# Optimization experiments

Hardware: AMD Instinct MI355X
Metric: run time of the kernel (lower is better)

## Reference

```python
import jax, jax.numpy as jnp
import numpy as np

N = 300000   # active voxels
K = 27       # 3^3 kernel offsets (kernel_size=3, D=3)
CIN = 64
COUT = 96
EPS = 1e-5   # MinkowskiBatchNorm default eps


def setup_inputs() -> dict:
    key = jax.random.key(0)
    ks = jax.random.split(key, 4)
    x = jax.random.normal(ks[0], (N, CIN), jnp.float32)
    nbrs = jax.random.randint(ks[1], (N, K), 0, N, jnp.int32)
    W1 = jax.random.normal(ks[2], (K, CIN, COUT), jnp.float32) * (1.0 / np.sqrt(K * CIN))
    W2 = jax.random.normal(ks[3], (K, COUT, COUT), jnp.float32) * (1.0 / np.sqrt(K * COUT))
    g1 = jnp.ones((COUT,), jnp.float32)
    b1 = jnp.zeros((COUT,), jnp.float32)
    g2 = jnp.ones((COUT,), jnp.float32)
    b2 = jnp.zeros((COUT,), jnp.float32)
    return {"x": x, "nbrs": nbrs, "W1": W1, "g1": g1, "b1": b1,
            "W2": W2, "g2": g2, "b2": b2}


def _sparse_conv(x, nbrs, W):
    # x: [N, Cin], nbrs: [N, K], W: [K, Cin, Cout]
    # Gather-GEMM-scatter with identical in/out coords (stride-1 3^D conv):
    # out[i] = sum_k x[nbrs[i,k]] @ W[k]. Scan over K to avoid the [N,K,Cin] blowup.
    acc0 = jnp.zeros((x.shape[0], W.shape[-1]), x.dtype)
    def step(acc, kw):
        nbr_k, W_k = kw
        return acc + x[nbr_k] @ W_k, None
    acc, _ = jax.lax.scan(step, acc0, (nbrs.T, W))
    return acc


def _bn_relu(h, gamma, beta):
    # training-mode batch norm over the point axis, then ReLU
    mu = jnp.mean(h, axis=0)
    var = jnp.var(h, axis=0)
    return jax.nn.relu((h - mu) * jax.lax.rsqrt(var + EPS) * gamma + beta)


def reference(x, nbrs, W1, g1, b1, W2, g2, b2):
    h = _bn_relu(_sparse_conv(x, nbrs, W1), g1, b1)
    return _bn_relu(_sparse_conv(h, nbrs, W2), g2, b2)
```

## Files before the change

### kernel.cpp

```cpp
#include <hip/hip_runtime.h>
#include <hip/hip_bf16.h>
#include <stdint.h>

#define N_VOX 300000
#define KNB   27
#define COUT  96
#define EPS   1e-5f
#define BM    256
#define NBLK  ((N_VOX + BM - 1) / BM)
#define QS_H  (255.0f / 6.0f)
#define XCLAMP 4.2f
#define QS_X  (127.0f / XCLAMP)

typedef __attribute__((ext_vector_type(8))) short  short8;
typedef __attribute__((ext_vector_type(4))) float  f32x4;
typedef __attribute__((ext_vector_type(4))) float  float4v;
typedef __attribute__((ext_vector_type(4))) unsigned short ushort4v;
typedef __attribute__((ext_vector_type(4))) int    int4v;
typedef __attribute__((ext_vector_type(2))) unsigned int uint2v;

__device__ __forceinline__ unsigned short f2bf(float f) {
    uint32_t u = __float_as_uint(f);
    uint32_t r = (u + 0x7FFFu + ((u >> 16) & 1u)) >> 16;
    return (unsigned short)r;
}
__device__ __forceinline__ float bf2f(unsigned short b) {
    return __uint_as_float(((uint32_t)b) << 16);
}

__device__ __forceinline__ void barrier_lgkm() {
    asm volatile("s_waitcnt lgkmcnt(0)" ::: "memory");
    __builtin_amdgcn_s_barrier();
    asm volatile("" ::: "memory");
}

__global__ void cast_xq_kernel(const float4v* __restrict__ x, int4v* __restrict__ xq, int n16) {
    int i = blockIdx.x * blockDim.x + threadIdx.x;
    int stride = gridDim.x * blockDim.x;
    for (; i < n16; i += stride) {
        int4v o;
#pragma unroll
        for (int g = 0; g < 4; ++g) {
            float4v v = x[i * 4 + g];
            unsigned int packed = 0;
#pragma unroll
            for (int j = 0; j < 4; ++j) {
                int q = (int)floorf(v[j] * QS_X + 0.5f);
                q = q > 127 ? 127 : (q < -127 ? -127 : q);
                packed |= ((unsigned int)(q & 0xff)) << (8 * j);
            }
            o[g] = (int)packed;
        }
        xq[i] = o;
    }
}

__global__ void wmax_kernel(const float* __restrict__ W, int n, unsigned int* __restrict__ wmax_bits) {
    int tid = threadIdx.x;
    float m = 0.f;
    for (int i = blockIdx.x * blockDim.x + tid; i < n; i += gridDim.x * blockDim.x)
        m = fmaxf(m, fabsf(W[i]));
#pragma unroll
    for (int off = 1; off <= 32; off <<= 1) m = fmaxf(m, __shfl_xor(m, off));
    __shared__ float red[4];
    int wid = tid >> 6;
    if ((tid & 63) == 0) red[wid] = m;
    __syncthreads();
    if (tid == 0) {
        m = fmaxf(fmaxf(red[0], red[1]), fmaxf(red[2], red[3]));
        atomicMax(wmax_bits, __float_as_uint(m));
    }
}

__device__ __forceinline__ int quant_w(float v, float qs) {
    int iv = (int)floorf(v * qs + 0.5f);
    return iv > 127 ? 127 : (iv < -127 ? -127 : iv);
}

__global__ void cast_w1q_kernel(const float* __restrict__ W1, signed char* __restrict__ W1q,
                                const unsigned int* __restrict__ wmax_bits, int total) {
    int idx = blockIdx.x * blockDim.x + threadIdx.x;
    if (idx >= total) return;
    float w1max = __uint_as_float(*wmax_bits);
    float qs = 16256.0f / w1max;
    int j    = idx & 15;
    int l    = (idx >> 4) & 63;
    int rest = idx >> 10;
    int p    = rest & 1;
    int cfk  = rest >> 1;
    int cf   = cfk % 6;
    int k    = cfk / 6;
    int ci   = ((l >> 4) << 4) + j;
    int co   = cf * 16 + (l & 15);
    float v = W1[(k * 64 + ci) * 96 + co] * qs;
    int wi = (int)floorf(v + 0.5f);
    wi = wi > 16256 ? 16256 : (wi < -16256 ? -16256 : wi);
    int hi = (wi + 64) >> 7;
    int lo = wi - (hi << 7);
    W1q[idx] = (signed char)(p == 0 ? hi : lo);
}

__global__ void cast_w2q_kernel(const float* __restrict__ W2, signed char* __restrict__ W2q,
                                const unsigned int* __restrict__ wmax_bits, int total) {
    int idx = blockIdx.x * blockDim.x + threadIdx.x;
    if (idx >= total) return;
    float wmax = __uint_as_float(*wmax_bits);
    float qs = 127.0f / wmax;
    int j  = idx & 15;
    int l  = (idx >> 4) & 63;
    int u  = (idx >> 10) & 1;
    int r2 = idx >> 11;
    int cf = r2 % 6;
    int k  = r2 / 6;
    int ci = 64 * u + ((l >> 4) << 4) + j;
    int co = cf * 16 + (l & 15);
    signed char q = 0;
    if (ci < 96) q = (signed char)quant_w(W2[(k * 96 + ci) * 96 + co], qs);
    W2q[idx] = q;
}

__global__ void colsumq_kernel(const float* __restrict__ W2,
                               const unsigned int* __restrict__ wmax_bits,
                               float* __restrict__ Ccorr) {
    int co  = blockIdx.x;
    int tid = threadIdx.x;
    float wmax = __uint_as_float(*wmax_bits);
    float qs = 127.0f / wmax;
    int s = 0;
    for (int e = tid; e < KNB * 96; e += 256)
        s += quant_w(W2[e * 96 + co], qs);
#pragma unroll
    for (int off = 1; off <= 32; off <<= 1) s += __shfl_xor(s, off);
    __shared__ int red[4];
    int wid = tid >> 6;
    if ((tid & 63) == 0) red[wid] = s;
    __syncthreads();
    if (tid == 0) {
        s = red[0] + red[1] + red[2] + red[3];
        float sw = (6.0f / 255.0f) * wmax / 127.0f;
        Ccorr[co] = 128.0f * sw * (float)s;
    }
}

__launch_bounds__(512, 4)
__global__ void conv1_i8_kernel(const signed char* __restrict__ Xq,
                                const int* __restrict__ nbrs,
                                const signed char* __restrict__ W1q,
                                const unsigned int* __restrict__ wmax_bits,
                                void* __restrict__ out,
                                float* __restrict__ partials) {
    __shared__ int nbr_s[BM * KNB];
    __shared__ __align__(16) signed char bbuf[2][12288];

    const int tid  = threadIdx.x;
    const int blk  = blockIdx.x;
    const int base = blk * BM;
    const int w    = tid >> 6;
    const int l    = tid & 63;
    const int lo   = l & 15;
    const int hi   = l >> 4;

    const float w1max = __uint_as_float(*wmax_bits);
    const float s1 = (XCLAMP / 127.0f) * (w1max / 16256.0f);

    for (int i = tid; i < BM * KNB; i += 512) {
        int gi = base * KNB + i;
        nbr_s[i] = (gi < N_VOX * KNB) ? nbrs[gi] : 0;
    }

    int4v acch[2][6], accl[2][6];
#pragma unroll
    for (int f = 0; f < 2; ++f)
#pragma unroll
        for (int cf = 0; cf < 6; ++cf) {
            acch[f][cf] = (int4v){0, 0, 0, 0};
            accl[f][cf] = (int4v){0, 0, 0, 0};
        }

    int4v a0[2], a1[2], stg[2];

    auto stage_load = [&](int k) {
        const signed char* src = W1q + (size_t)k * 12288;
#pragma unroll
        for (int n = 0; n < 2; ++n) {
            int c = w + n * 8;
            if (c < 12)
                stg[n] = *(const int4v*)(src + c * 1024 + l * 16);
        }
    };
    auto stage_write = [&](signed char* buf) {
#pragma unroll
        for (int n = 0; n < 2; ++n) {
            int c = w + n * 8;
            if (c < 12)
                *(int4v*)&buf[c * 1024 + l * 16] = stg[n];
        }
    };
    auto loadA = [&](int k, int4v (&a)[2]) {
#pragma unroll
        for (int f = 0; f < 2; ++f) {
            int v   = w * 32 + f * 16 + lo;
            int row = nbr_s[v * KNB + k];
            a[f] = *(const int4v*)(Xq + (size_t)row * 64 + hi * 16);
        }
    };
    auto mfmaP = [&](const signed char* buf, int4v (&a)[2]) {
#pragma unroll
        for (int cf = 0; cf < 6; ++cf) {
            int4v bh = *(const int4v*)&buf[(cf * 2 + 0) * 1024 + l * 16];
            int4v bl = *(const int4v*)&buf[(cf * 2 + 1) * 1024 + l * 16];
#pragma unroll
            for (int f = 0; f < 2; ++f) {
                acch[f][cf] = __builtin_amdgcn_mfma_i32_16x16x64_i8(a[f], bh, acch[f][cf], 0, 0, 0);
                accl[f][cf] = __builtin_amdgcn_mfma_i32_16x16x64_i8(a[f], bl, accl[f][cf], 0, 0, 0);
            }
        }
    };

    stage_load(0);
    __syncthreads();
    stage_write(bbuf[0]);
    loadA(0, a0);
    __syncthreads();

#pragma unroll 1
    for (int kk = 0; kk < KNB - 1; kk += 2) {
        stage_load(kk + 1);
        loadA(kk + 1, a1);
        mfmaP(bbuf[0], a0);
        stage_write(bbuf[1]);
        barrier_lgkm();
        stage_load(kk + 2);
        loadA(kk + 2, a0);
        mfmaP(bbuf[1], a1);
        stage_write(bbuf[0]);
        barrier_lgkm();
    }
    mfmaP(bbuf[0], a0);
    __syncthreads();

    float s_sum[6], s_sq[6];
#pragma unroll
    for (int cf = 0; cf < 6; ++cf) { s_sum[cf] = 0.f; s_sq[cf] = 0.f; }

#pragma unroll
    for (int f = 0; f < 2; ++f) {
        int m0 = base + w * 32 + f * 16 + hi * 4;
#pragma unroll
        for (int i = 0; i < 4; ++i) {
            int m = m0 + i;
            bool valid = (m < N_VOX);
#pragma unroll
            for (int cf = 0; cf < 6; ++cf) {
                int comb = (acch[f][cf][i] << 7) + accl[f][cf][i];
                float val = s1 * (float)comb;
                int col = cf * 16 + lo;
                if (valid) {
                    ((unsigned short*)out)[(size_t)m * COUT + col] = f2bf(val);
                    s_sum[cf] += val;
                    s_sq[cf]  += val * val;
                }
            }
        }
    }

    float* stat = (float*)bbuf;
#pragma unroll
    for (int cf = 0; cf < 6; ++cf) {
        float s = s_sum[cf], q = s_sq[cf];
        s += __shfl_xor(s, 16); q += __shfl_xor(q, 16);
        s += __shfl_xor(s, 32); q += __shfl_xor(q, 32);
        if (hi == 0) {
            stat[w * 192 + cf * 16 + lo]        = s;
            stat[w * 192 + COUT + cf * 16 + lo] = q;
        }
    }
    __syncthreads();
    if (tid < 2 * COUT) {
        float v = 0.f;
#pragma unroll
        for (int ww = 0; ww < 8; ++ww) v += stat[ww * 192 + tid];
        partials[blk * (2 * COUT) + tid] = v;
    }
}

template <bool OUT_BF16>
__launch_bounds__(512, 4)
__global__ void conv2_i8_kernel(const signed char* __restrict__ H8,
                                const int* __restrict__ nbrs,
                                const signed char* __restrict__ W2q,
                                const unsigned int* __restrict__ wmax_bits,
                                const float* __restrict__ Ccorr,
                                void* __restrict__ out,
                                float* __restrict__ partials) {
    __shared__ int nbr_s[BM * KNB];
    __shared__ __align__(16) signed char bbuf[2][12288];

    const int tid  = threadIdx.x;
    const int blk  = blockIdx.x;
    const int base = blk * BM;
    const int w    = tid >> 6;
    const int l    = tid & 63;
    const int lo   = l & 15;
    const int hi   = l >> 4;

    const float wmax = __uint_as_float(*wmax_bits);
    const float sw   = (6.0f / 255.0f) * wmax / 127.0f;

    for (int i = tid; i < BM * KNB; i += 512) {
        int gi = base * KNB + i;
        nbr_s[i] = (gi < N_VOX * KNB) ? nbrs[gi] : 0;
    }

    int4v acc[2][6];
#pragma unroll
    for (int f = 0; f < 2; ++f)
#pragma unroll
        for (int cf = 0; cf < 6; ++cf)
            acc[f][cf] = (int4v){0, 0, 0, 0};

    int4v a0[2][2], a1[2][2], stg[2];

    auto stage_load = [&](int k) {
        const signed char* src = W2q + (size_t)k * 12288;
#pragma unroll
        for (int n = 0; n < 2; ++n) {
            int c = w + n * 8;
            if (c < 12)
                stg[n] = *(const int4v*)(src + c * 1024 + l * 16);
        }
    };
    auto stage_write = [&](signed char* buf) {
#pragma unroll
        for (int n = 0; n < 2; ++n) {
            int c = w + n * 8;
            if (c < 12)
                *(int4v*)&buf[c * 1024 + l * 16] = stg[n];
        }
    };
    auto loadA = [&](int k, int4v (&a)[2][2]) {
#pragma unroll
        for (int f = 0; f < 2; ++f) {
            int v   = w * 32 + f * 16 + lo;
            int row = nbr_s[v * KNB + k];
            const signed char* hp = H8 + (size_t)row * 96;
            a[f][0] = *(const int4v*)(hp + hi * 16);
            a[f][1] = (hi < 2) ? *(const int4v*)(hp + 64 + hi * 16)
                               : (int4v){0, 0, 0, 0};
        }
    };
    auto mfmaP = [&](const signed char* buf, int4v (&a)[2][2]) {
#pragma unroll
        for (int cf = 0; cf < 6; ++cf)
#pragma unroll
            for (int u = 0; u < 2; ++u) {
                int4v b = *(const int4v*)&buf[(cf * 2 + u) * 1024 + l * 16];
                acc[0][cf] = __builtin_amdgcn_mfma_i32_16x16x64_i8(a[0][u], b, acc[0][cf], 0, 0, 0);
                acc[1][cf] = __builtin_amdgcn_mfma_i32_16x16x64_i8(a[1][u], b, acc[1][cf], 0, 0, 0);
            }
    };

    stage_load(0);
    __syncthreads();
    stage_write(bbuf[0]);
    loadA(0, a0);
    __syncthreads();

#pragma unroll 1
    for (int kk = 0; kk < KNB - 1; kk += 2) {
        stage_load(kk + 1);
        loadA(kk + 1, a1);
        mfmaP(bbuf[0], a0);
        stage_write(bbuf[1]);
        barrier_lgkm();
        stage_load(kk + 2);
        loadA(kk + 2, a0);
        mfmaP(bbuf[1], a1);
        stage_write(bbuf[0]);
        barrier_lgkm();
    }
    mfmaP(bbuf[0], a0);
    __syncthreads();

    float cc[6];
#pragma unroll
    for (int cf = 0; cf < 6; ++cf) cc[cf] = Ccorr[cf * 16 + lo];

    float s_sum[6], s_sq[6];
#pragma unroll
    for (int cf = 0; cf < 6; ++cf) { s_sum[cf] = 0.f; s_sq[cf] = 0.f; }

#pragma unroll
    for (int f = 0; f < 2; ++f) {
        int m0 = base + w * 32 + f * 16 + hi * 4;
#pragma unroll
        for (int i = 0; i < 4; ++i) {
            int m = m0 + i;
            bool valid = (m < N_VOX);
#pragma unroll
            for (int cf = 0; cf < 6; ++cf) {
                float val = sw * (float)acc[f][cf][i] + cc[cf];
                int col = cf * 16 + lo;
                if (valid) {
                    if (OUT_BF16) ((unsigned short*)out)[(size_t)m * COUT + col] = f2bf(val);
                    else          ((float*)out)[(size_t)m * COUT + col] = val;
                    s_sum[cf] += val;
                    s_sq[cf]  += val * val;
                }
            }
        }
    }

    float* stat = (float*)bbuf;
#pragma unroll
    for (int cf = 0; cf < 6; ++cf) {
        float s = s_sum[cf], q = s_sq[cf];
        s += __shfl_xor(s, 16); q += __shfl_xor(q, 16);
        s += __shfl_xor(s, 32); q += __shfl_xor(q, 32);
        if (hi == 0) {
            stat[w * 192 + cf * 16 + lo]        = s;
            stat[w * 192 + COUT + cf * 16 + lo] = q;
        }
    }
    __syncthreads();
    if (tid < 2 * COUT) {
        float v = 0.f;
#pragma unroll
        for (int ww = 0; ww < 8; ++ww) v += stat[ww * 192 + tid];
        partials[blk * (2 * COUT) + tid] = v;
    }
}

__global__ void finalize_kernel(const float* __restrict__ partials, int nblk,
                                const float* __restrict__ gamma, const float* __restrict__ beta,
                                float* __restrict__ scale, float* __restrict__ bias) {
    int c = blockIdx.x;
    int tid = threadIdx.x;
    float s = 0.f, q = 0.f;
    for (int b = tid; b < nblk; b += 256) {
        s += partials[b * 192 + c];
        q += partials[b * 192 + 96 + c];
    }
    __shared__ float rs[4], rq[4];
#pragma unroll
    for (int m = 1; m <= 32; m <<= 1) { s += __shfl_xor(s, m); q += __shfl_xor(q, m); }
    int wid = tid >> 6, lane = tid & 63;
    if (lane == 0) { rs[wid] = s; rq[wid] = q; }
    __syncthreads();
    if (tid == 0) {
        s = rs[0] + rs[1] + rs[2] + rs[3];
        q = rq[0] + rq[1] + rq[2] + rq[3];
        float mu  = s / (float)N_VOX;
        float var = q / (float)N_VOX - mu * mu;
        float rsg = rsqrtf(var + EPS);
        float sc  = gamma[c] * rsg;
        scale[c] = sc;
        bias[c]  = beta[c] - mu * sc;
    }
}

__global__ void bnrelu_quant_kernel(const unsigned short* __restrict__ h,
                                    const float* __restrict__ scale,
                                    const float* __restrict__ bias,
                                    signed char* __restrict__ h8, int n8) {
    __shared__ float sc[COUT], bi[COUT];
    if (threadIdx.x < COUT) { sc[threadIdx.x] = scale[threadIdx.x]; bi[threadIdx.x] = bias[threadIdx.x]; }
    __syncthreads();
    int i = blockIdx.x * blockDim.x + threadIdx.x;
    int stride = gridDim.x * blockDim.x;
    for (; i < n8; i += stride) {
        int e  = i * 8;
        int c0 = e % COUT;
        short8 v = *(const short8*)(h + e);
        unsigned int w0 = 0, w1 = 0;
#pragma unroll
        for (int j = 0; j < 4; ++j) {
            float f0 = fmaxf(bf2f((unsigned short)v[j])     * sc[c0 + j]     + bi[c0 + j], 0.f);
            float f1 = fmaxf(bf2f((unsigned short)v[j + 4]) * sc[c0 + j + 4] + bi[c0 + j + 4], 0.f);
            int q0 = (int)(f0 * QS_H + 0.5f) - 128; q0 = q0 > 127 ? 127 : q0;
            int q1 = (int)(f1 * QS_H + 0.5f) - 128; q1 = q1 > 127 ? 127 : q1;
            w0 |= ((unsigned int)(q0 & 0xff)) << (8 * j);
            w1 |= ((unsigned int)(q1 & 0xff)) << (8 * j);
        }
        uint2v o = {w0, w1};
        *(uint2v*)(h8 + e) = o;
    }
}

__global__ void bnrelu_bf16_to_f32_kernel(const unsigned short* __restrict__ y,
                                          const float* __restrict__ scale,
                                          const float* __restrict__ bias,
                                          float* __restrict__ out, int n8) {
    __shared__ float sc[COUT], bi[COUT];
    if (threadIdx.x < COUT) { sc[threadIdx.x] = scale[threadIdx.x]; bi[threadIdx.x] = bias[threadIdx.x]; }
    __syncthreads();
    int i = blockIdx.x * blockDim.x + threadIdx.x;
    int stride = gridDim.x * blockDim.x;
    for (; i < n8; i += stride) {
        int e  = i * 8;
        int c0 = e % COUT;
        short8 v = *(const short8*)(y + e);
        float4v o0, o1;
#pragma unroll
        for (int j = 0; j < 4; ++j) {
            o0[j] = fmaxf(bf2f((unsigned short)v[j])     * sc[c0 + j]     + bi[c0 + j], 0.f);
            o1[j] = fmaxf(bf2f((unsigned short)v[j + 4]) * sc[c0 + j + 4] + bi[c0 + j + 4], 0.f);
        }
        *(float4v*)(out + e)     = o0;
        *(float4v*)(out + e + 4) = o1;
    }
}

__global__ void bnrelu_f32_kernel(float* __restrict__ h,
                                  const float* __restrict__ scale,
                                  const float* __restrict__ bias, int total) {
    __shared__ float sc[COUT], bi[COUT];
    if (threadIdx.x < COUT) { sc[threadIdx.x] = scale[threadIdx.x]; bi[threadIdx.x] = bias[threadIdx.x]; }
    __syncthreads();
    int i = blockIdx.x * blockDim.x + threadIdx.x;
    int stride = gridDim.x * blockDim.x;
    for (; i < total; i += stride) {
        int c = i % COUT;
        float v = h[i] * sc[c] + bi[c];
        h[i] = fmaxf(v, 0.f);
    }
}

extern "C" void kernel_launch(void* const* d_in, const int* in_sizes, int n_in,
                              void* d_out, int out_size, void* d_ws, size_t ws_size,
                              hipStream_t stream) {
    const float* x    = (const float*)d_in[0];
    const int*   nbrs = (const int*)  d_in[1];
    const float* W1   = (const float*)d_in[2];
    const float* g1   = (const float*)d_in[3];
    const float* b1   = (const float*)d_in[4];
    const float* W2   = (const float*)d_in[5];
    const float* g2   = (const float*)d_in[6];
    const float* b2   = (const float*)d_in[7];

    char* ws = (char*)d_ws;
    signed char*    xq  = (signed char*)(ws);
    float*          p2  = (float*)(ws + 19200000);
    signed char*    h8  = (signed char*)(ws + 21000192);
    unsigned short* h0  = (unsigned short*)(ws + 50000128);
    signed char*    w1q = (signed char*)(ws + 107600128);
    signed char*    w2q = (signed char*)(ws + 107931904);
    float* p1    = (float*)(ws + 108263680);
    float* sb    = (float*)(ws + 110063872);
    float* scale1 = sb;
    float* bias1  = sb + 96;
    float* scale2 = sb + 192;
    float* bias2  = sb + 288;
    unsigned int* wmax2_bits = (unsigned int*)(sb + 384);
    unsigned int* wmax1_bits = wmax2_bits + 1;
    float* Ccorr = sb + 448;
    unsigned short* yraw = (unsigned short*)(ws + 110067968);

    const bool use_yraw = (ws_size >= (size_t)110067968 + 57600000);

    hipMemsetAsync(wmax2_bits, 0, 8, stream);
    wmax_kernel<<<96, 256, 0, stream>>>(W2, KNB * 96 * 96, wmax2_bits);
    wmax_kernel<<<64, 256, 0, stream>>>(W1, KNB * 64 * 96, wmax1_bits);
    cast_w1q_kernel<<<(331776 + 255) / 256, 256, 0, stream>>>(W1, w1q, wmax1_bits, 331776);
    cast_w2q_kernel<<<(331776 + 255) / 256, 256, 0, stream>>>(W2, w2q, wmax2_bits, 331776);
    colsumq_kernel<<<96, 256, 0, stream>>>(W2, wmax2_bits, Ccorr);

    cast_xq_kernel<<<2048, 256, 0, stream>>>((const float4v*)x, (int4v*)xq, N_VOX * 64 / 16);

    conv1_i8_kernel<<<NBLK, 512, 0, stream>>>(xq, nbrs, w1q, wmax1_bits, h0, p1);

    finalize_kernel<<<96, 256, 0, stream>>>(p1, NBLK, g1, b1, scale1, bias1);
    bnrelu_quant_kernel<<<4096, 256, 0, stream>>>(h0, scale1, bias1, h8, N_VOX * COUT / 8);

    if (use_yraw) {
        conv2_i8_kernel<true><<<NBLK, 512, 0, stream>>>(h8, nbrs, w2q, wmax2_bits, Ccorr, yraw, p2);
        finalize_kernel<<<96, 256, 0, stream>>>(p2, NBLK, g2, b2, scale2, bias2);
        bnrelu_bf16_to_f32_kernel<<<8192, 256, 0, stream>>>(yraw, scale2, bias2,
                                                            (float*)d_out, N_VOX * COUT / 8);
    } else {
        conv2_i8_kernel<false><<<NBLK, 512, 0, stream>>>(h8, nbrs, w2q, wmax2_bits, Ccorr, d_out, p2);
        finalize_kernel<<<96, 256, 0, stream>>>(p2, NBLK, g2, b2, scale2, bias2);
        bnrelu_f32_kernel<<<2048, 256, 0, stream>>>((float*)d_out, scale2, bias2, N_VOX * COUT);
    }
}
```

Before: 555.6 us.

## Deepen A-operand prefetch and stage conv1 output through LDS for coalesced stores

The conv1 kernel now prefetches gathered A fragments two kernel offsets ahead using four register sets, so gather latency gets more MFMA work to hide behind. Its bf16 output is first written to a padded LDS tile and then copied to global memory as 16-byte coalesced rows, instead of scattered 2-byte stores. This costs extra registers, which may hurt occupancy under the launch bounds, plus an additional barrier and shared-memory pass.

```diff
diff --git a/kernel.cpp b/kernel.cpp
--- a/kernel.cpp
+++ b/kernel.cpp
@@ -147,10 +147,11 @@
                                 const int* __restrict__ nbrs,
                                 const signed char* __restrict__ W1q,
                                 const unsigned int* __restrict__ wmax_bits,
-                                void* __restrict__ out,
+                                unsigned short* __restrict__ out,
                                 float* __restrict__ partials) {
-    __shared__ int nbr_s[BM * KNB];
-    __shared__ __align__(16) signed char bbuf[2][12288];
+    __shared__ __align__(16) char smem[52224];
+    int* nbr_s = (int*)smem;
+    signed char (*bbuf)[12288] = (signed char (*)[12288])(smem + 27648);
 
     const int tid  = threadIdx.x;
     const int blk  = blockIdx.x;
@@ -177,7 +178,7 @@
             accl[f][cf] = (int4v){0, 0, 0, 0};
         }
 
-    int4v a0[2], a1[2], stg[2];
+    int4v aA[2], aB[2], aC[2], aD[2], stg[2];
 
     auto stage_load = [&](int k) {
         const signed char* src = W1q + (size_t)k * 12288;
@@ -220,51 +221,42 @@
     stage_load(0);
     __syncthreads();
     stage_write(bbuf[0]);
-    loadA(0, a0);
+    loadA(0, aA);
+    loadA(1, aB);
     __syncthreads();
 
 #pragma unroll 1
-    for (int kk = 0; kk < KNB - 1; kk += 2) {
-        stage_load(kk + 1);
-        loadA(kk + 1, a1);
-        mfmaP(bbuf[0], a0);
-        stage_write(bbuf[1]);
-        barrier_lgkm();
-        stage_load(kk + 2);
-        loadA(kk + 2, a0);
-        mfmaP(bbuf[1], a1);
-        stage_write(bbuf[0]);
-        barrier_lgkm();
-    }
-    mfmaP(bbuf[0], a0);
+    for (int kk = 0; kk < 24; kk += 4) {
+        stage_load(kk + 1); loadA(kk + 2, aC); mfmaP(bbuf[0], aA); stage_write(bbuf[1]); barrier_lgkm();
+        stage_load(kk + 2); loadA(kk + 3, aD); mfmaP(bbuf[1], aB); stage_write(bbuf[0]); barrier_lgkm();
+        stage_load(kk + 3); loadA(kk + 4, aA); mfmaP(bbuf[0], aC); stage_write(bbuf[1]); barrier_lgkm();
+        stage_load(kk + 4); loadA(kk + 5, aB); mfmaP(bbuf[1], aD); stage_write(bbuf[0]); barrier_lgkm();
+    }
+    stage_load(25); loadA(26, aC); mfmaP(bbuf[0], aA); stage_write(bbuf[1]); barrier_lgkm();
+    stage_load(26);                mfmaP(bbuf[1], aB); stage_write(bbuf[0]); barrier_lgkm();
+    mfmaP(bbuf[0], aC);
     __syncthreads();
 
     float s_sum[6], s_sq[6];
 #pragma unroll
     for (int cf = 0; cf < 6; ++cf) { s_sum[cf] = 0.f; s_sq[cf] = 0.f; }
-
 #pragma unroll
     for (int f = 0; f < 2; ++f) {
         int m0 = base + w * 32 + f * 16 + hi * 4;
 #pragma unroll
         for (int i = 0; i < 4; ++i) {
-            int m = m0 + i;
-            bool valid = (m < N_VOX);
-#pragma unroll
-            for (int cf = 0; cf < 6; ++cf) {
-                int comb = (acch[f][cf][i] << 7) + accl[f][cf][i];
-                float val = s1 * (float)comb;
-                int col = cf * 16 + lo;
-                if (valid) {
-                    ((unsigned short*)out)[(size_t)m * COUT + col] = f2bf(val);
+            if (m0 + i < N_VOX) {
+#pragma unroll
+                for (int cf = 0; cf < 6; ++cf) {
+                    int comb = (acch[f][cf][i] << 7) + accl[f][cf][i];
+                    float val = s1 * (float)comb;
                     s_sum[cf] += val;
                     s_sq[cf]  += val * val;
                 }
             }
         }
     }
-
-    float* stat = (float*)bbuf;
+    float* stat = (float*)(smem + 27648);
 #pragma unroll
     for (int cf = 0; cf < 6; ++cf) {
         float s = s_sum[cf], q = s_sq[cf];
@@ -281,6 +273,32 @@
 #pragma unroll
         for (int ww = 0; ww < 8; ++ww) v += stat[ww * 192 + tid];
         partials[blk * (2 * COUT) + tid] = v;
+    }
+    __syncthreads();
+
+    unsigned short* ostage = (unsigned short*)smem;
+#pragma unroll
+    for (int f = 0; f < 2; ++f) {
+        int r0 = w * 32 + f * 16 + hi * 4;
+#pragma unroll
+        for (int i = 0; i < 4; ++i) {
+#pragma unroll
+            for (int cf = 0; cf < 6; ++cf) {
+                int comb = (acch[f][cf][i] << 7) + accl[f][cf][i];
+                ostage[(r0 + i) * 100 + cf * 16 + lo] = f2bf(s1 * (float)comb);
+            }
+        }
+    }
+    __syncthreads();
+
+    char* gout = (char*)out + (size_t)base * 192;
+    for (int c = tid; c < 3072; c += 512) {
+        int row = c / 12;
+        int off = c - row * 12;
+        if (base + row < N_VOX) {
+            int4v v = *(const int4v*)((const char*)ostage + row * 200 + off * 16);
+            *(int4v*)(gout + c * 16) = v;
+        }
     }
 }
 
```

After: 933.4 us. +68.0%, slower.
